# Performance work log

Hardware: AMD Instinct MI355X
Metric: run time of the kernel (lower is better)

The kernel has to match this reference:

```python
import jax, jax.numpy as jnp
import numpy as np

N_NODES = 20000


def _gcn_conv(x, edge_index, W, b):
    """PyG GCNConv: add self-loops, symmetric normalization, x @ W, scatter-add, + bias."""
    n = x.shape[0]
    loops = jnp.arange(n, dtype=edge_index.dtype)
    src = jnp.concatenate([edge_index[0], loops])  # [E+N]
    dst = jnp.concatenate([edge_index[1], loops])  # [E+N]
    # degree of target nodes (edge weight 1), self-loops guarantee deg >= 1
    deg = jax.ops.segment_sum(jnp.ones_like(dst, dtype=x.dtype), dst, num_segments=n)
    dinv = jax.lax.rsqrt(deg)
    norm = dinv[src] * dinv[dst]  # [E+N]
    h = x @ W  # [n, out] dense GEMM before aggregation (standard GCNConv ordering)
    msg = h[src] * norm[:, None]  # gather + scale over edges
    out = jax.ops.segment_sum(msg, dst, num_segments=n)  # scatter-add to targets
    return out + b


def setup_inputs() -> dict:
    key = jax.random.key(0)
    k = jax.random.split(key, 6)
    in_f, h_f, n_cls = 512, 512, 256
    x = jax.random.normal(k[0], (N_NODES, in_f), dtype=jnp.float32)
    edge_index = jax.random.randint(k[1], (2, 160000), 0, N_NODES, dtype=jnp.int64)
    W1 = jax.random.normal(k[2], (in_f, h_f), dtype=jnp.float32) * (1.0 / np.sqrt(in_f))
    b1 = jnp.zeros((h_f,), dtype=jnp.float32)
    W2 = jax.random.normal(k[3], (h_f, n_cls), dtype=jnp.float32) * (1.0 / np.sqrt(h_f))
    b2 = jnp.zeros((n_cls,), dtype=jnp.float32)
    return {"x": x, "edge_index": edge_index, "W1": W1, "b1": b1, "W2": W2, "b2": b2}


def reference(x, edge_index, W1, b1, W2, b2):
    h = jax.nn.relu(_gcn_conv(x, edge_index, W1, b1))
    h = jax.nn.relu(_gcn_conv(h, edge_index, W2, b2))
    # F.dropout in eval mode is identity; reference is deterministic eval-mode forward
    return h
```

## Files before the change

kernel.cpp:

```cpp
#include <hip/hip_runtime.h>


typedef __bf16 bf16x8 __attribute__((ext_vector_type(8)));
typedef float floatx4 __attribute__((ext_vector_type(4)));
typedef unsigned short ushort_t;
typedef unsigned int uint_t;

#define MAXD 32
#define CAP 40

__device__ inline ushort_t f2bf(float f) {
    unsigned u = __builtin_bit_cast(unsigned, f);
    unsigned r = (u + 0x7FFFu + ((u >> 16) & 1u)) >> 16;
    return (ushort_t)r;
}
__device__ inline float bf_lo(uint_t u) { return __builtin_bit_cast(float, u << 16); }
__device__ inline float bf_hi(uint_t u) { return __builtin_bit_cast(float, u & 0xFFFF0000u); }
__device__ inline uint_t pk2(float lo, float hi) {
    return (uint_t)f2bf(lo) | ((uint_t)f2bf(hi) << 16);
}

__device__ inline void transpose_tile(const float* __restrict__ in,
                                      ushort_t* __restrict__ out,
                                      int K, int N, int k0, int n0,
                                      ushort_t (*tile)[33]) {
    int tx = threadIdx.x & 31, ty = threadIdx.x >> 5;
    for (int r = ty; r < 32; r += 8)
        tile[r][tx] = f2bf(in[(size_t)(k0 + r) * N + n0 + tx]);
    __syncthreads();
    for (int r = ty; r < 32; r += 8)
        out[(size_t)(n0 + r) * K + k0 + tx] = tile[tx][r];
}

__global__ __launch_bounds__(256) void prep_fused(
    const int* __restrict__ src, const int* __restrict__ dst,
    int* __restrict__ deg, int* __restrict__ col_ell,
    int* __restrict__ ovf_cnt, int* __restrict__ ovf, int e, int nb_e,
    const float* __restrict__ x, ushort_t* __restrict__ xb, long xcount, int nb_conv,
    const float* __restrict__ W1, ushort_t* __restrict__ w1t,
    const float* __restrict__ W2, ushort_t* __restrict__ w2t) {
    __shared__ ushort_t tile[32][33];
    int b = blockIdx.x;
    if (b < nb_e) {
        int i = b * 256 + threadIdx.x;
        if (i < e) {
            int s = src[i], d = dst[i];
            int slot = atomicAdd(&deg[d], 1);
            if (slot < MAXD) {
                col_ell[d * MAXD + slot] = s;
            } else {
                int k = atomicAdd(ovf_cnt, 1);
                ovf[2 * k] = d;
                ovf[2 * k + 1] = s;
            }
        }
        return;
    }
    b -= nb_e;
    if (b < nb_conv) {
        long i = ((long)b * 256 + threadIdx.x) * 4;
        if (i < xcount) {
            float4 v = *(const float4*)(x + i);
            ushort4 o = make_ushort4(f2bf(v.x), f2bf(v.y), f2bf(v.z), f2bf(v.w));
            *(ushort4*)(xb + i) = o;
        }
        return;
    }
    b -= nb_conv;
    if (b < 256) {
        transpose_tile(W1, w1t, 512, 512, (b >> 4) * 32, (b & 15) * 32, tile);
        return;
    }
    b -= 256;
    transpose_tile(W2, w2t, 512, 256, (b >> 3) * 32, (b & 7) * 32, tile);
}

__global__ __launch_bounds__(256) void gemm_mfma(
    const ushort_t* __restrict__ A, const ushort_t* __restrict__ BT,
    ushort_t* __restrict__ C,
    int M, int N, int K, int nbx, int gemm_blocks,
    const int* __restrict__ deg, float* __restrict__ dinv_out, int n) {
    __shared__ __align__(16) ushort_t As[8192];
    __shared__ __align__(16) ushort_t Bs[8192];

    if ((int)blockIdx.x >= gemm_blocks) {
        int i = ((int)blockIdx.x - gemm_blocks) * 256 + threadIdx.x;
        if (i < n) dinv_out[i] = 1.0f / sqrtf((float)(deg[i] + 1));
        return;
    }

    const int bx = (int)blockIdx.x % nbx, by = (int)blockIdx.x / nbx;
    const int tid = threadIdx.x;
    const int w = tid >> 6, lane = tid & 63;
    const int q = lane >> 4, ml = lane & 15;
    const int wm = (w >> 1) * 64, wn = (w & 1) * 64;
    const int row0 = by * 128, col0 = bx * 128;

    const int rr = lane >> 3;
    const int gsw = (lane & 7) ^ (rr & 7);
    const ushort_t* ga[4];
    const ushort_t* gb[4];
    ushort_t* la[4];
    ushort_t* lb[4];
#pragma unroll
    for (int rp = 0; rp < 4; rp++) {
        int r = rp * 32 + w * 8 + rr;
        int gra = min(row0 + r, M - 1);
        ga[rp] = A + (size_t)gra * K + gsw * 8;
        gb[rp] = BT + (size_t)(col0 + r) * K + gsw * 8;
        la[rp] = As + rp * 2048 + w * 512;
        lb[rp] = Bs + rp * 2048 + w * 512;
    }

    const int sel = ml & 7;
    int aoff[2][4], boff[2][4];
#pragma unroll
    for (int st = 0; st < 2; st++)
#pragma unroll
        for (int i = 0; i < 4; i++) {
            int g = q + st * 4;
            aoff[st][i] = (wm + i * 16 + ml) * 64 + ((g ^ sel) << 3);
            boff[st][i] = (wn + i * 16 + ml) * 64 + ((g ^ sel) << 3);
        }

    floatx4 acc[4][4];
#pragma unroll
    for (int i = 0; i < 4; i++)
#pragma unroll
        for (int j = 0; j < 4; j++) acc[i][j] = (floatx4)0.0f;

    for (int kt = 0; kt < K; kt += 64) {
#pragma unroll
        for (int rp = 0; rp < 4; rp++) {
            __builtin_amdgcn_global_load_lds(
                (const __attribute__((address_space(1))) unsigned*)ga[rp],
                (__attribute__((address_space(3))) unsigned*)la[rp], 16, 0, 0);
            __builtin_amdgcn_global_load_lds(
                (const __attribute__((address_space(1))) unsigned*)gb[rp],
                (__attribute__((address_space(3))) unsigned*)lb[rp], 16, 0, 0);
            ga[rp] += 64; gb[rp] += 64;
        }
        __syncthreads();
#pragma unroll
        for (int st = 0; st < 2; st++) {
            bf16x8 af[4], bfr[4];
#pragma unroll
            for (int i = 0; i < 4; i++) {
                af[i] = *(const bf16x8*)(As + aoff[st][i]);
                bfr[i] = *(const bf16x8*)(Bs + boff[st][i]);
            }
#pragma unroll
            for (int i = 0; i < 4; i++)
#pragma unroll
                for (int j = 0; j < 4; j++)
                    acc[i][j] = __builtin_amdgcn_mfma_f32_16x16x32_bf16(
                        af[i], bfr[j], acc[i][j], 0, 0, 0);
        }
        __syncthreads();
    }

#pragma unroll
    for (int i = 0; i < 4; i++) {
        int rbase = row0 + wm + i * 16 + q * 4;
#pragma unroll
        for (int j = 0; j < 4; j++) {
            int gc = col0 + wn + j * 16 + ml;
#pragma unroll
            for (int r = 0; r < 4; r++) {
                int gr = rbase + r;
                if (gr < M) C[(size_t)gr * N + gc] = f2bf(acc[i][j][r]);
            }
        }
    }
}

__global__ __launch_bounds__(256, 2) void gemm2_fused(
    const ushort_t* __restrict__ g,
    const ushort_t* __restrict__ BT,
    const int* __restrict__ deg, const int* __restrict__ col_ell,
    const int* __restrict__ ovf_cnt, const int* __restrict__ ovf,
    const float* __restrict__ dinv, const float* __restrict__ b1,
    ushort_t* __restrict__ g2, int M) {
    __shared__ __align__(16) ushort_t As[64 * 64];
    __shared__ __align__(16) ushort_t Bs[256 * 64];
    __shared__ int   cols_s[64][CAP];
    __shared__ float ps_s[64][CAP];
    __shared__ float b1_s[512];
    __shared__ short cnt_s[64];

    const int tid = threadIdx.x;
    const int w = tid >> 6, lane = tid & 63;
    const int q = lane >> 4, ml = lane & 15;
    const int wn = w * 64;
    const int row0 = (int)blockIdx.x * 64;

    for (int i = tid; i < 512; i += 256) b1_s[i] = b1[i];
    {
        int r = tid >> 2, jj = tid & 3;
        int rg = min(row0 + r, M - 1);
        int cnt = min(deg[rg], MAXD);
        float pd = dinv[rg];
        if (jj == 0) {
            cols_s[r][0] = rg;
            ps_s[r][0] = pd;
            cnt_s[r] = (short)(cnt + 1);
        }
        const int* cm = col_ell + (size_t)rg * MAXD;
        for (int j = jj; j < CAP - 1; j += 4) {
            bool vld = j < cnt;
            int c = vld ? cm[j] : rg;
            cols_s[r][j + 1] = c;
            ps_s[r][j + 1] = vld ? dinv[c] : 0.0f;
        }
    }
    const int nov = *ovf_cnt;

    const int rr = lane >> 3;
    const int gsw = (lane & 7) ^ (rr & 7);
    const ushort_t* gb[8];
    ushort_t* lb[8];
#pragma unroll
    for (int rp = 0; rp < 8; rp++) {
        gb[rp] = BT + (size_t)(rp * 32 + w * 8 + rr) * 512 + gsw * 8;
        lb[rp] = Bs + rp * 2048 + w * 512;
    }

    const int sel = ml & 7;
    int aoff[2][4], boff[2][4];
#pragma unroll
    for (int st = 0; st < 2; st++)
#pragma unroll
        for (int i = 0; i < 4; i++) {
            int gg = q + st * 4;
            aoff[st][i] = (i * 16 + ml) * 64 + ((gg ^ sel) << 3);
            boff[st][i] = (wn + i * 16 + ml) * 64 + ((gg ^ sel) << 3);
        }

    floatx4 acc[4][4];
#pragma unroll
    for (int i = 0; i < 4; i++)
#pragma unroll
        for (int j = 0; j < 4; j++) acc[i][j] = (floatx4)0.0f;

    const int ar = tid >> 3;
    const int kg = tid & 7;

    __syncthreads();

    for (int kt = 0; kt < 512; kt += 64) {
#pragma unroll
        for (int rp = 0; rp < 8; rp++) {
            __builtin_amdgcn_global_load_lds(
                (const __attribute__((address_space(1))) unsigned*)gb[rp],
                (__attribute__((address_space(3))) unsigned*)lb[rp], 16, 0, 0);
            gb[rp] += 64;
        }

        const ushort_t* gk = g + kt + kg * 8;
#pragma unroll
        for (int p = 0; p < 2; p++) {
            const int r = ar + p * 32;
            const int cntR = (int)cnt_s[r];
            const float pdr = ps_s[r][0];
            float a[8];
#pragma unroll
            for (int k = 0; k < 8; k++) a[k] = 0.0f;
            for (int e0 = 0; e0 < cntR; e0 += 8) {
                uint4 u[8];
                float ps[8];
#pragma unroll
                for (int j = 0; j < 8; j++) {
                    int s = cols_s[r][e0 + j];
                    ps[j] = ps_s[r][e0 + j];
                    u[j] = *(const uint4*)(gk + (size_t)s * 512);
                }
#pragma unroll
                for (int j = 0; j < 8; j++) {
                    a[0] = fmaf(ps[j], bf_lo(u[j].x), a[0]);
                    a[1] = fmaf(ps[j], bf_hi(u[j].x), a[1]);
                    a[2] = fmaf(ps[j], bf_lo(u[j].y), a[2]);
                    a[3] = fmaf(ps[j], bf_hi(u[j].y), a[3]);
                    a[4] = fmaf(ps[j], bf_lo(u[j].z), a[4]);
                    a[5] = fmaf(ps[j], bf_hi(u[j].z), a[5]);
                    a[6] = fmaf(ps[j], bf_lo(u[j].w), a[6]);
                    a[7] = fmaf(ps[j], bf_hi(u[j].w), a[7]);
                }
            }
            for (int k2 = 0; k2 < nov; k2++) {
                if (ovf[2 * k2] == cols_s[r][0]) {
                    int s = ovf[2 * k2 + 1];
                    float ps = dinv[s];
                    uint4 u = *(const uint4*)(gk + (size_t)s * 512);
                    a[0] = fmaf(ps, bf_lo(u.x), a[0]);
                    a[1] = fmaf(ps, bf_hi(u.x), a[1]);
                    a[2] = fmaf(ps, bf_lo(u.y), a[2]);
                    a[3] = fmaf(ps, bf_hi(u.y), a[3]);
                    a[4] = fmaf(ps, bf_lo(u.z), a[4]);
                    a[5] = fmaf(ps, bf_hi(u.z), a[5]);
                    a[6] = fmaf(ps, bf_lo(u.w), a[6]);
                    a[7] = fmaf(ps, bf_hi(u.w), a[7]);
                }
            }
            float4 bv0 = *(const float4*)(b1_s + kt + kg * 8);
            float4 bv1 = *(const float4*)(b1_s + kt + kg * 8 + 4);
            float h0 = fmaxf(fmaf(pdr, a[0], bv0.x), 0.0f);
            float h1 = fmaxf(fmaf(pdr, a[1], bv0.y), 0.0f);
            float h2 = fmaxf(fmaf(pdr, a[2], bv0.z), 0.0f);
            float h3 = fmaxf(fmaf(pdr, a[3], bv0.w), 0.0f);
            float h4 = fmaxf(fmaf(pdr, a[4], bv1.x), 0.0f);
            float h5 = fmaxf(fmaf(pdr, a[5], bv1.y), 0.0f);
            float h6 = fmaxf(fmaf(pdr, a[6], bv1.z), 0.0f);
            float h7 = fmaxf(fmaf(pdr, a[7], bv1.w), 0.0f);
            uint4 U;
            U.x = pk2(h0, h1);
            U.y = pk2(h2, h3);
            U.z = pk2(h4, h5);
            U.w = pk2(h6, h7);
            *(uint4*)(As + r * 64 + ((kg ^ (r & 7)) << 3)) = U;
        }
        __syncthreads();

#pragma unroll
        for (int st = 0; st < 2; st++) {
            bf16x8 af[4], bfr[4];
#pragma unroll
            for (int i = 0; i < 4; i++) {
                af[i] = *(const bf16x8*)(As + aoff[st][i]);
                bfr[i] = *(const bf16x8*)(Bs + boff[st][i]);
            }
#pragma unroll
            for (int i = 0; i < 4; i++)
#pragma unroll
                for (int j = 0; j < 4; j++)
                    acc[i][j] = __builtin_amdgcn_mfma_f32_16x16x32_bf16(
                        af[i], bfr[j], acc[i][j], 0, 0, 0);
        }
        __syncthreads();
    }

#pragma unroll
    for (int i = 0; i < 4; i++) {
        int rbase = row0 + i * 16 + q * 4;
        float pd4[4];
#pragma unroll
        for (int r = 0; r < 4; r++)
            pd4[r] = (rbase + r < M) ? dinv[rbase + r] : 1.0f;
#pragma unroll
        for (int j = 0; j < 4; j++) {
            int gc = wn + j * 16 + ml;
#pragma unroll
            for (int r = 0; r < 4; r++) {
                int gr = rbase + r;
                if (gr < M) g2[(size_t)gr * 256 + gc] = f2bf(pd4[r] * acc[i][j][r]);
            }
        }
    }
}

__global__ __launch_bounds__(64) void aggregate2(const uint2* __restrict__ g,
                                                 const int* __restrict__ deg,
                                                 const int* __restrict__ col_ell,
                                                 const int* __restrict__ ovf_cnt,
                                                 const int* __restrict__ ovf,
                                                 const float* __restrict__ dinv,
                                                 const float* __restrict__ bias,
                                                 float* __restrict__ out) {
    const int d = blockIdx.x, t = threadIdx.x;
    const int cnt = min(deg[d], MAXD);
    const float pd = dinv[d];
    const size_t base = (size_t)d * 64 + t;
    const int* cm = col_ell + (size_t)d * MAXD;

    int cv = 0;
    float wv = 0.0f;
    if (t < MAXD && t < cnt) {
        cv = cm[t];
        wv = 1.0f;
    }
    float4 b = *(const float4*)(bias + t * 4);

    uint2 us = g[base];
    float a0 = bf_lo(us.x), a1 = bf_hi(us.x);
    float a2 = bf_lo(us.y), a3 = bf_hi(us.y);

    for (int e0 = 0; e0 < cnt; e0 += 8) {
        uint2 u[8];
        float ws[8];
#pragma unroll
        for (int j = 0; j < 8; j++) {
            int s = __shfl(cv, e0 + j);
            ws[j] = __shfl(wv, e0 + j);
            u[j] = g[(size_t)s * 64 + t];
        }
#pragma unroll
        for (int j = 0; j < 8; j++) {
            a0 = fmaf(ws[j], bf_lo(u[j].x), a0);
            a1 = fmaf(ws[j], bf_hi(u[j].x), a1);
            a2 = fmaf(ws[j], bf_lo(u[j].y), a2);
            a3 = fmaf(ws[j], bf_hi(u[j].y), a3);
        }
    }
    int nov = *ovf_cnt;
    for (int k = 0; k < nov; k++) {
        if (ovf[2 * k] == d) {
            uint2 u = g[(size_t)ovf[2 * k + 1] * 64 + t];
            a0 += bf_lo(u.x); a1 += bf_hi(u.x);
            a2 += bf_lo(u.y); a3 += bf_hi(u.y);
        }
    }
    float4 o;
    o.x = fmaxf(fmaf(pd, a0, b.x), 0.0f);
    o.y = fmaxf(fmaf(pd, a1, b.y), 0.0f);
    o.z = fmaxf(fmaf(pd, a2, b.z), 0.0f);
    o.w = fmaxf(fmaf(pd, a3, b.w), 0.0f);
    *(float4*)(out + (size_t)d * 256 + t * 4) = o;
}

extern "C" void kernel_launch(void* const* d_in, const int* in_sizes, int n_in,
                              void* d_out, int out_size, void* d_ws, size_t ws_size,
                              hipStream_t stream) {
    const float* x  = (const float*)d_in[0];
    const int*   ei = (const int*)d_in[1];
    const float* W1 = (const float*)d_in[2];
    const float* b1 = (const float*)d_in[3];
    const float* W2 = (const float*)d_in[4];
    const float* b2 = (const float*)d_in[5];
    float* out = (float*)d_out;

    const int FIN = 512, FH = 512, FOUT = 256;
    const int n = in_sizes[0] / FIN;
    const int e = in_sizes[1] / 2;
    const int* src = ei;
    const int* dst = ei + e;

    auto align_up = [](size_t v) { return (v + 255) & ~(size_t)255; };
    char* w = (char*)d_ws;
    int*      deg     = (int*)w;
    int*      ovf_cnt = deg + n;
    w += align_up((size_t)(n + 1) * 4);
    float*    dinv    = (float*)w;    w += align_up((size_t)n * 4);
    int*      col_ell = (int*)w;      w += align_up((size_t)n * MAXD * 4);
    int*      ovf     = (int*)w;      w += align_up((size_t)2048 * 4);
    ushort_t* xb      = (ushort_t*)w; w += align_up((size_t)n * FIN * 2);
    ushort_t* w1t     = (ushort_t*)w; w += align_up((size_t)FH * FIN * 2);
    ushort_t* w2t     = (ushort_t*)w; w += align_up((size_t)FOUT * FH * 2);
    ushort_t* g       = (ushort_t*)w; w += align_up((size_t)n * FH * 2);
    ushort_t* g2      = (ushort_t*)w; w += align_up((size_t)n * FH * 2);

    const int nb_n = (n + 255) / 256;
    const int nb_e = (e + 255) / 256;
    const long xcount = (long)n * FIN;
    const int nb_conv = (int)((xcount / 4 + 255) / 256);

    hipMemsetAsync(deg, 0, (size_t)(n + 1) * 4, stream);

    prep_fused<<<nb_e + nb_conv + 256 + 128, 256, 0, stream>>>(
        src, dst, deg, col_ell, ovf_cnt, ovf, e, nb_e,
        x, xb, xcount, nb_conv, W1, w1t, W2, w2t);

    {
        const int mb = (n + 127) / 128;
        int gemm_blocks = (FH / 128) * mb;
        gemm_mfma<<<gemm_blocks + nb_n, 256, 0, stream>>>(
            xb, w1t, g, n, FH, FIN, FH / 128, gemm_blocks, deg, dinv, n);
    }
    gemm2_fused<<<(n + 63) / 64, 256, 0, stream>>>(
        g, w2t, deg, col_ell, ovf_cnt, ovf, dinv, b1, g2, n);

    aggregate2<<<n, 64, 0, stream>>>((const uint2*)g2, deg, col_ell, ovf_cnt,
                                     ovf, dinv, b2, out);

    (void)ws_size; (void)n_in; (void)out_size;
}
```

Before: 199.0 us.

## Shrink fused agg1+GEMM2 tile to 16 rows for more blocks and parallel gathers

The fused layer-1 aggregation plus layer-2 GEMM kernel now processes 16 rows per block instead of 64. This gives about 1250 blocks instead of about 313 to fill the GPU better. Each thread gathers 4 features of one row instead of 8 features of two rows sequentially, and neighbour index and weight pairs are packed into one int2 LDS array. The cost is that the full 256x512 W2 tile is streamed into LDS four times as often per row, and each MFMA pass has less reuse (one A fragment per four B fragments).

```diff
diff --git a/kernel.cpp b/kernel.cpp
--- a/kernel.cpp
+++ b/kernel.cpp
@@ -174,43 +174,47 @@
     }
 }
 
-__global__ __launch_bounds__(256, 2) void gemm2_fused(
+__global__ __launch_bounds__(256) void agg1gemm2(
     const ushort_t* __restrict__ g,
     const ushort_t* __restrict__ BT,
     const int* __restrict__ deg, const int* __restrict__ col_ell,
     const int* __restrict__ ovf_cnt, const int* __restrict__ ovf,
     const float* __restrict__ dinv, const float* __restrict__ b1,
     ushort_t* __restrict__ g2, int M) {
-    __shared__ __align__(16) ushort_t As[64 * 64];
+    __shared__ __align__(16) ushort_t As[16 * 64];
     __shared__ __align__(16) ushort_t Bs[256 * 64];
-    __shared__ int   cols_s[64][CAP];
-    __shared__ float ps_s[64][CAP];
+    __shared__ int2  adj_s[16][CAP];
     __shared__ float b1_s[512];
-    __shared__ short cnt_s[64];
+    __shared__ int   cnt_s[16];
 
     const int tid = threadIdx.x;
     const int w = tid >> 6, lane = tid & 63;
     const int q = lane >> 4, ml = lane & 15;
     const int wn = w * 64;
-    const int row0 = (int)blockIdx.x * 64;
+    const int row0 = (int)blockIdx.x * 16;
 
     for (int i = tid; i < 512; i += 256) b1_s[i] = b1[i];
     {
-        int r = tid >> 2, jj = tid & 3;
+        int r = tid >> 4, jj = tid & 15;
         int rg = min(row0 + r, M - 1);
         int cnt = min(deg[rg], MAXD);
-        float pd = dinv[rg];
-        if (jj == 0) {
-            cols_s[r][0] = rg;
-            ps_s[r][0] = pd;
-            cnt_s[r] = (short)(cnt + 1);
-        }
         const int* cm = col_ell + (size_t)rg * MAXD;
-        for (int j = jj; j < CAP - 1; j += 4) {
-            bool vld = j < cnt;
-            int c = vld ? cm[j] : rg;
-            cols_s[r][j + 1] = c;
-            ps_s[r][j + 1] = vld ? dinv[c] : 0.0f;
+#pragma unroll
+        for (int pass = 0; pass < 3; pass++) {
+            int j = jj + pass * 16;
+            if (j >= CAP) break;
+            int2 a;
+            if (j == 0) {
+                a.x = rg;
+                a.y = __builtin_bit_cast(int, dinv[rg]);
+                cnt_s[r] = cnt + 1;
+            } else {
+                bool vld = (j - 1) < cnt;
+                int c = vld ? cm[j - 1] : rg;
+                a.x = c;
+                a.y = vld ? __builtin_bit_cast(int, dinv[c]) : 0;
+            }
+            adj_s[r][j] = a;
         }
     }
     const int nov = *ovf_cnt;
@@ -226,26 +230,27 @@
     }
 
     const int sel = ml & 7;
-    int aoff[2][4], boff[2][4];
-#pragma unroll
-    for (int st = 0; st < 2; st++)
-#pragma unroll
-        for (int i = 0; i < 4; i++) {
-            int gg = q + st * 4;
-            aoff[st][i] = (i * 16 + ml) * 64 + ((gg ^ sel) << 3);
+    int aoff[2], boff[2][4];
+#pragma unroll
+    for (int st = 0; st < 2; st++) {
+        int gg = q + st * 4;
+        aoff[st] = ml * 64 + ((gg ^ sel) << 3);
+#pragma unroll
+        for (int i = 0; i < 4; i++)
             boff[st][i] = (wn + i * 16 + ml) * 64 + ((gg ^ sel) << 3);
-        }
-
-    floatx4 acc[4][4];
-#pragma unroll
-    for (int i = 0; i < 4; i++)
-#pragma unroll
-        for (int j = 0; j < 4; j++) acc[i][j] = (floatx4)0.0f;
-
-    const int ar = tid >> 3;
-    const int kg = tid & 7;
+    }
+
+    floatx4 acc[4];
+#pragma unroll
+    for (int j = 0; j < 4; j++) acc[j] = (floatx4)0.0f;
+
+    const int gr_ = tid >> 4;
+    const int fc = tid & 15;
 
     __syncthreads();
+    const int cntR = cnt_s[gr_];
+    const float pdr = __builtin_bit_cast(float, adj_s[gr_][0].y);
+    const int selfR = adj_s[gr_][0].x;
 
     for (int kt = 0; kt < 512; kt += 64) {
 #pragma unroll
@@ -256,102 +261,71 @@
             gb[rp] += 64;
         }
 
-        const ushort_t* gk = g + kt + kg * 8;
-#pragma unroll
-        for (int p = 0; p < 2; p++) {
-            const int r = ar + p * 32;
-            const int cntR = (int)cnt_s[r];
-            const float pdr = ps_s[r][0];
-            float a[8];
-#pragma unroll
-            for (int k = 0; k < 8; k++) a[k] = 0.0f;
-            for (int e0 = 0; e0 < cntR; e0 += 8) {
-                uint4 u[8];
-                float ps[8];
-#pragma unroll
-                for (int j = 0; j < 8; j++) {
-                    int s = cols_s[r][e0 + j];
-                    ps[j] = ps_s[r][e0 + j];
-                    u[j] = *(const uint4*)(gk + (size_t)s * 512);
-                }
-#pragma unroll
-                for (int j = 0; j < 8; j++) {
-                    a[0] = fmaf(ps[j], bf_lo(u[j].x), a[0]);
-                    a[1] = fmaf(ps[j], bf_hi(u[j].x), a[1]);
-                    a[2] = fmaf(ps[j], bf_lo(u[j].y), a[2]);
-                    a[3] = fmaf(ps[j], bf_hi(u[j].y), a[3]);
-                    a[4] = fmaf(ps[j], bf_lo(u[j].z), a[4]);
-                    a[5] = fmaf(ps[j], bf_hi(u[j].z), a[5]);
-                    a[6] = fmaf(ps[j], bf_lo(u[j].w), a[6]);
-                    a[7] = fmaf(ps[j], bf_hi(u[j].w), a[7]);
-                }
-            }
-            for (int k2 = 0; k2 < nov; k2++) {
-                if (ovf[2 * k2] == cols_s[r][0]) {
-                    int s = ovf[2 * k2 + 1];
-                    float ps = dinv[s];
-                    uint4 u = *(const uint4*)(gk + (size_t)s * 512);
-                    a[0] = fmaf(ps, bf_lo(u.x), a[0]);
-                    a[1] = fmaf(ps, bf_hi(u.x), a[1]);
-                    a[2] = fmaf(ps, bf_lo(u.y), a[2]);
-                    a[3] = fmaf(ps, bf_hi(u.y), a[3]);
-                    a[4] = fmaf(ps, bf_lo(u.z), a[4]);
-                    a[5] = fmaf(ps, bf_hi(u.z), a[5]);
-                    a[6] = fmaf(ps, bf_lo(u.w), a[6]);
-                    a[7] = fmaf(ps, bf_hi(u.w), a[7]);
-                }
-            }
-            float4 bv0 = *(const float4*)(b1_s + kt + kg * 8);
-            float4 bv1 = *(const float4*)(b1_s + kt + kg * 8 + 4);
-            float h0 = fmaxf(fmaf(pdr, a[0], bv0.x), 0.0f);
-            float h1 = fmaxf(fmaf(pdr, a[1], bv0.y), 0.0f);
-            float h2 = fmaxf(fmaf(pdr, a[2], bv0.z), 0.0f);
-            float h3 = fmaxf(fmaf(pdr, a[3], bv0.w), 0.0f);
-            float h4 = fmaxf(fmaf(pdr, a[4], bv1.x), 0.0f);
-            float h5 = fmaxf(fmaf(pdr, a[5], bv1.y), 0.0f);
-            float h6 = fmaxf(fmaf(pdr, a[6], bv1.z), 0.0f);
-            float h7 = fmaxf(fmaf(pdr, a[7], bv1.w), 0.0f);
-            uint4 U;
-            U.x = pk2(h0, h1);
-            U.y = pk2(h2, h3);
-            U.z = pk2(h4, h5);
-            U.w = pk2(h6, h7);
-            *(uint4*)(As + r * 64 + ((kg ^ (r & 7)) << 3)) = U;
-        }
+        const ushort_t* gk = g + kt + fc * 4;
+        float a0 = 0.0f, a1 = 0.0f, a2 = 0.0f, a3 = 0.0f;
+        for (int e0 = 0; e0 < cntR; e0 += 8) {
+            uint2 u[8];
+            float ps[8];
+#pragma unroll
+            for (int j = 0; j < 8; j++) {
+                int2 cp = adj_s[gr_][e0 + j];
+                ps[j] = __builtin_bit_cast(float, cp.y);
+                u[j] = *(const uint2*)(gk + (size_t)cp.x * 512);
+            }
+#pragma unroll
+            for (int j = 0; j < 8; j++) {
+                a0 = fmaf(ps[j], bf_lo(u[j].x), a0);
+                a1 = fmaf(ps[j], bf_hi(u[j].x), a1);
+                a2 = fmaf(ps[j], bf_lo(u[j].y), a2);
+                a3 = fmaf(ps[j], bf_hi(u[j].y), a3);
+            }
+        }
+        for (int k2 = 0; k2 < nov; k2++) {
+            if (ovf[2 * k2] == selfR) {
+                int s = ovf[2 * k2 + 1];
+                float ps = dinv[s];
+                uint2 u = *(const uint2*)(gk + (size_t)s * 512);
+                a0 = fmaf(ps, bf_lo(u.x), a0);
+                a1 = fmaf(ps, bf_hi(u.x), a1);
+                a2 = fmaf(ps, bf_lo(u.y), a2);
+                a3 = fmaf(ps, bf_hi(u.y), a3);
+            }
+        }
+        float4 bv = *(const float4*)(b1_s + kt + fc * 4);
+        float h0 = fmaxf(fmaf(pdr, a0, bv.x), 0.0f);
+        float h1 = fmaxf(fmaf(pdr, a1, bv.y), 0.0f);
+        float h2 = fmaxf(fmaf(pdr, a2, bv.z), 0.0f);
+        float h3 = fmaxf(fmaf(pdr, a3, bv.w), 0.0f);
+        uint2 U;
+        U.x = pk2(h0, h1);
+        U.y = pk2(h2, h3);
+        *(uint2*)(As + gr_ * 64 + (((fc >> 1) ^ (gr_ & 7)) << 3) + (fc & 1) * 4) = U;
+
         __syncthreads();
 
 #pragma unroll
         for (int st = 0; st < 2; st++) {
-            bf16x8 af[4], bfr[4];
-#pragma unroll
-            for (int i = 0; i < 4; i++) {
-                af[i] = *(const bf16x8*)(As + aoff[st][i]);
-                bfr[i] = *(const bf16x8*)(Bs + boff[st][i]);
-            }
-#pragma unroll
-            for (int i = 0; i < 4; i++)
-#pragma unroll
-                for (int j = 0; j < 4; j++)
-                    acc[i][j] = __builtin_amdgcn_mfma_f32_16x16x32_bf16(
-                        af[i], bfr[j], acc[i][j], 0, 0, 0);
+            bf16x8 af = *(const bf16x8*)(As + aoff[st]);
+#pragma unroll
+            for (int j = 0; j < 4; j++) {
+                bf16x8 bfr = *(const bf16x8*)(Bs + boff[st][j]);
+                acc[j] = __builtin_amdgcn_mfma_f32_16x16x32_bf16(af, bfr, acc[j],
+                                                                 0, 0, 0);
+            }
         }
         __syncthreads();
     }
 
 #pragma unroll
-    for (int i = 0; i < 4; i++) {
-        int rbase = row0 + i * 16 + q * 4;
-        float pd4[4];
-#pragma unroll
-        for (int r = 0; r < 4; r++)
-            pd4[r] = (rbase + r < M) ? dinv[rbase + r] : 1.0f;
-#pragma unroll
-        for (int j = 0; j < 4; j++) {
-            int gc = wn + j * 16 + ml;
-#pragma unroll
-            for (int r = 0; r < 4; r++) {
-                int gr = rbase + r;
-                if (gr < M) g2[(size_t)gr * 256 + gc] = f2bf(pd4[r] * acc[i][j][r]);
+    for (int j = 0; j < 4; j++) {
+        int gc = wn + j * 16 + ml;
+#pragma unroll
+        for (int r = 0; r < 4; r++) {
+            int lrow = q * 4 + r;
+            int grow = row0 + lrow;
+            if (grow < M) {
+                float pd = __builtin_bit_cast(float, adj_s[lrow][0].y);
+                g2[(size_t)grow * 256 + gc] = f2bf(pd * acc[j][r]);
             }
         }
     }
@@ -445,7 +419,7 @@
     ushort_t* w1t     = (ushort_t*)w; w += align_up((size_t)FH * FIN * 2);
     ushort_t* w2t     = (ushort_t*)w; w += align_up((size_t)FOUT * FH * 2);
     ushort_t* g       = (ushort_t*)w; w += align_up((size_t)n * FH * 2);
-    ushort_t* g2      = (ushort_t*)w; w += align_up((size_t)n * FH * 2);
+    ushort_t* g2      = (ushort_t*)w; w += align_up((size_t)n * FOUT * 2);
 
     const int nb_n = (n + 255) / 256;
     const int nb_e = (e + 255) / 256;
@@ -464,7 +438,7 @@
         gemm_mfma<<<gemm_blocks + nb_n, 256, 0, stream>>>(
             xb, w1t, g, n, FH, FIN, FH / 128, gemm_blocks, deg, dinv, n);
     }
-    gemm2_fused<<<(n + 63) / 64, 256, 0, stream>>>(
+    agg1gemm2<<<(n + 15) / 16, 256, 0, stream>>>(
         g, w2t, deg, col_ell, ovf_cnt, ovf, dinv, b1, g2, n);
 
     aggregate2<<<n, 64, 0, stream>>>((const uint2*)g2, deg, col_ell, ovf_cnt,
```

New measurement: 190.6 us. 4.2% less time.
